# Kernel tuning notes

Measured on AMD Instinct MI355X. Metric: run time of the kernel, lower is better.

The kernel has to match this reference:

```python
import jax, jax.numpy as jnp
import numpy as np

N = 1147      # 240 lncRNA + 412 disease + 495 miRNA nodes (hard-coded in source)
HID = 512
NH = 8        # heads
P = 73408     # edges (avg degree ~64)
IN_CH = 512


def _ln(x, eps=1e-5):
    m = x.mean(-1, keepdims=True)
    v = ((x - m) ** 2).mean(-1, keepdims=True)
    return (x - m) * jax.lax.rsqrt(v + eps)


def _seg_softmax_agg(logits, v_src, dst, n):
    # logits: [P, NH], v_src: [P, NH, d]; softmax over incoming edges per dst node
    m = jax.ops.segment_max(logits, dst, num_segments=n)
    m = jnp.where(jnp.isfinite(m), m, 0.0)
    a = jnp.exp(logits - m[dst])
    den = jax.ops.segment_sum(a, dst, num_segments=n)
    w = a / (den[dst] + 1e-9)
    return jax.ops.segment_sum(w[..., None] * v_src, dst, num_segments=n)


def _lap_pe(src, dst, n, k):
    # symmetric normalized Laplacian eigenvector positional encoding
    A = jnp.zeros((n, n), jnp.float32).at[src, dst].set(1.0)
    A = jnp.maximum(A, A.T)
    dinv = jax.lax.rsqrt(jnp.maximum(A.sum(1), 1.0))
    L = jnp.eye(n, dtype=jnp.float32) - dinv[:, None] * A * dinv[None, :]
    _, vecs = jnp.linalg.eigh(L)
    return vecs[:, 1:k + 1]  # drop trivial eigenvector


def _edge_layer(h, e, src, dst, Wq, Wk, Wv, We, Wo, Woe, Wfa, Wfb, Wea, Web):
    n, D = h.shape
    d = D // NH
    scale = 1.0 / np.sqrt(d)
    q = (h @ Wq).reshape(n, NH, d)
    k = (h @ Wk).reshape(n, NH, d)
    v = (h @ Wv).reshape(n, NH, d)
    ep = (e @ We).reshape(-1, NH, d)
    score = k[src] * q[dst] * scale * ep           # [P, NH, d]
    e1 = _ln(e + score.reshape(-1, D) @ Woe)       # edge residual path
    e1 = _ln(e1 + jax.nn.relu(e1 @ Wea) @ Web)
    agg = _seg_softmax_agg(score.sum(-1), v[src], dst, n).reshape(n, D)
    h1 = _ln(h + agg @ Wo)
    h1 = _ln(h1 + jax.nn.relu(h1 @ Wfa) @ Wfb)
    return h1, e1


def _gt_layer(h, src, dst, Wq, Wk, Wv, Wo, Wfa, Wfb):
    n, D = h.shape
    d = D // NH
    scale = 1.0 / np.sqrt(d)
    q = (h @ Wq).reshape(n, NH, d)
    k = (h @ Wk).reshape(n, NH, d)
    v = (h @ Wv).reshape(n, NH, d)
    logits = (k[src] * q[dst]).sum(-1) * scale     # [P, NH]
    agg = _seg_softmax_agg(logits, v[src], dst, n).reshape(n, D)
    h1 = _ln(h + agg @ Wo)
    h1 = _ln(h1 + jax.nn.relu(h1 @ Wfa) @ Wfb)
    return h1


def setup_inputs() -> dict:
    key = jax.random.key(0)
    ks = jax.random.split(key, 32)
    s = 0.02
    w = lambda i, shp: jax.random.normal(ks[i], shp, jnp.float32) * s
    return {
        'H': jax.random.normal(ks[0], (N, 1147), jnp.float32),
        'edge_w': jax.random.uniform(ks[1], (P, 1), jnp.float32),
        'edge_src': jax.random.randint(ks[2], (P,), 0, N, jnp.int32),
        'edge_dst': jax.random.randint(ks[3], (P,), 0, N, jnp.int32),
        'W_lin': w(4, (1147, IN_CH)), 'b_lin': jnp.zeros((IN_CH,), jnp.float32),
        'W_e': w(5, (1, HID)), 'b_e': jnp.zeros((HID,), jnp.float32),
        'W_h': w(6, (IN_CH, HID)), 'b_h': jnp.zeros((HID,), jnp.float32),
        'W_lap': w(7, (HID, HID)), 'b_lap': jnp.zeros((HID,), jnp.float32),
        'Wq1': w(8, (HID, HID)), 'Wk1': w(9, (HID, HID)), 'Wv1': w(10, (HID, HID)),
        'We1': w(11, (HID, HID)), 'Wo1': w(12, (HID, HID)), 'Woe1': w(13, (HID, HID)),
        'Wf1a': w(14, (HID, 2 * HID)), 'Wf1b': w(15, (2 * HID, HID)),
        'We1a': w(16, (HID, 2 * HID)), 'We1b': w(17, (2 * HID, HID)),
        'Wq2': w(18, (HID, HID)), 'Wk2': w(19, (HID, HID)), 'Wv2': w(20, (HID, HID)),
        'Wo2': w(21, (HID, HID)),
        'Wf2a': w(22, (HID, 2 * HID)), 'Wf2b': w(23, (2 * HID, HID)),
    }


def reference(H, edge_w, W_lin, b_lin, W_e, b_e, W_h, b_h, W_lap, b_lap,
              Wq1, Wk1, Wv1, We1, Wo1, Woe1, Wf1a, Wf1b, We1a, We1b,
              Wq2, Wk2, Wv2, Wo2, Wf2a, Wf2b, edge_src, edge_dst):
    e = edge_w @ W_e + b_e                       # embedding_e on edge weights
    h = (H @ W_lin + b_lin) @ W_h + b_h          # linear(1147->in_ch) then embedding_h
    pe = _lap_pe(edge_src, edge_dst, N, HID)     # laplacian positional encoding
    h = h + pe @ W_lap + b_lap
    z, _ = _edge_layer(h, e, edge_src, edge_dst, Wq1, Wk1, Wv1, We1,
                       Wo1, Woe1, Wf1a, Wf1b, We1a, We1b)
    z = _gt_layer(z, edge_src, edge_dst, Wq2, Wk2, Wv2, Wo2, Wf2a, Wf2b)
    return z  # [N, HID], already flat per node
```

## Files before the change

kernel.cpp:

```cpp
#include <hip/hip_runtime.h>
#include <hip/hip_cooperative_groups.h>
#include <math.h>

#define NN 1147
#define HID 512
#define LDAe 1152
#define LDQ 1152
#define LDD 1147
#define EPS32 5.9604644775390625e-08f
#define SAFMIN32 1.17549435e-38f
#define I0E 1026
#define TGRID 64
#define TBLK 1024

struct EDMeta { int K; int nrot; int early; float rho; };
struct ETree { int st[64]; int sz[64]; int cnt; };
struct MergeLvl { int cnt; int st[32]; int n1[32]; int n2[32]; };

__device__ __forceinline__ float lapy2f(float x, float y){
  float xa=fabsf(x), ya=fabsf(y), w=fmaxf(xa,ya), z2=fminf(xa,ya);
  if (z2==0.f) return w;
  float q=z2/w; return w*sqrtf(1.f+q*q);
}
__device__ __forceinline__ void slartg(float ff, float gg, float* c, float* s, float* r){
  if (gg==0.f){ *c=1.f; *s=0.f; *r=ff; }
  else if (ff==0.f){ *c=0.f; *s=copysignf(1.f,gg); *r=fabsf(gg); }
  else {
    float d=sqrtf(ff*ff+gg*gg);
    *c=fabsf(ff)/d;
    *r=copysignf(d,ff);
    *s=gg/(*r);
  }
}
__device__ void slaev2(float a, float b, float cc, float* rt1, float* rt2, float* cs1, float* sn1){
  float sm=a+cc, df=a-cc, adf=fabsf(df), tb=b+b, ab=fabsf(tb);
  float acmx, acmn;
  if (fabsf(a)>fabsf(cc)){ acmx=a; acmn=cc; } else { acmx=cc; acmn=a; }
  float rt;
  if (adf>ab) rt=adf*sqrtf(1.f+(ab/adf)*(ab/adf));
  else if (adf<ab) rt=ab*sqrtf(1.f+(adf/ab)*(adf/ab));
  else rt=ab*sqrtf(2.f);
  int sgn1;
  if (sm<0.f){ *rt1=0.5f*(sm-rt); sgn1=-1; *rt2=(acmx/(*rt1))*acmn-(b/(*rt1))*b; }
  else if (sm>0.f){ *rt1=0.5f*(sm+rt); sgn1=1; *rt2=(acmx/(*rt1))*acmn-(b/(*rt1))*b; }
  else { *rt1=0.5f*rt; *rt2=-0.5f*rt; sgn1=1; }
  int sgn2; float cs;
  if (df>=0.f){ cs=df+rt; sgn2=1; } else { cs=df-rt; sgn2=-1; }
  float acs=fabsf(cs);
  if (acs>ab){ float ct=-tb/cs; *sn1=1.f/sqrtf(1.f+ct*ct); *cs1=ct*(*sn1); }
  else {
    if (ab==0.f){ *cs1=1.f; *sn1=0.f; }
    else { float tn=-cs/tb; *cs1=1.f/sqrtf(1.f+tn*tn); *sn1=tn*(*cs1); }
  }
  if (sgn1==sgn2){ float tn=*cs1; *cs1=-(*sn1); *sn1=tn; }
}
__device__ void lamrg0(int n1,int n2,const float* a,int dtrd1,int dtrd2,int* idx){
  int n1sv=n1,n2sv=n2;
  int ind1=(dtrd1>0)?0:(n1-1);
  int ind2=(dtrd2>0)?n1:(n1+n2-1);
  int i=0;
  while(n1sv>0&&n2sv>0){
    if(a[ind1]<=a[ind2]){idx[i++]=ind1;ind1+=dtrd1;n1sv--;}
    else{idx[i++]=ind2;ind2+=dtrd2;n2sv--;}
  }
  while(n2sv>0){idx[i++]=ind2;ind2+=dtrd2;n2sv--;}
  while(n1sv>0){idx[i++]=ind1;ind1+=dtrd1;n1sv--;}
}

__global__ __launch_bounds__(256) void k_zero_f(float* p, int n){
  int i = blockIdx.x*256+threadIdx.x; if (i<n) p[i]=0.f;
}
__global__ __launch_bounds__(256) void k_zero_i(int* p, int n){
  int i = blockIdx.x*256+threadIdx.x; if (i<n) p[i]=0;
}

__global__ __launch_bounds__(256) void k_adj(const int* __restrict__ src, const int* __restrict__ dst,
                                             float* __restrict__ A, int P){
  int p = blockIdx.x*256+threadIdx.x;
  if (p>=P) return;
  int s=src[p], d=dst[p];
  A[(size_t)s*LDAe+d]=1.f;
  A[(size_t)d*LDAe+s]=1.f;
}
__global__ __launch_bounds__(256) void k_deg(const float* __restrict__ A, float* __restrict__ dinv){
  int row=blockIdx.x; int tid=threadIdx.x;
  __shared__ float red[256];
  float s=0.f;
  for (int c=tid;c<NN;c+=256) s+=A[(size_t)row*LDAe+c];
  red[tid]=s; __syncthreads();
  for(int st=128;st;st>>=1){ if(tid<st) red[tid]+=red[tid+st]; __syncthreads(); }
  if(tid==0) dinv[row]=1.f/sqrtf(fmaxf(red[0],1.f));
}
__global__ __launch_bounds__(256) void k_lap(float* __restrict__ A, const float* __restrict__ dinv){
  int row=blockIdx.y; int col=blockIdx.x*256+threadIdx.x;
  if (col>=NN) return;
  size_t idx=(size_t)row*LDAe+col;
  float v=A[idx];
  float v1=(dinv[row]*v)*dinv[col];
  float v2=(dinv[col]*v)*dinv[row];
  A[idx] = ((row==col)?1.f:0.f) - 0.5f*(v1+v2);
}

__device__ __forceinline__ float dload(const float* p){
  return __hip_atomic_load(p, __ATOMIC_RELAXED, __HIP_MEMORY_SCOPE_AGENT);
}
__device__ __forceinline__ void dstore(float* p, float v){
  __hip_atomic_store(p, v, __ATOMIC_RELAXED, __HIP_MEMORY_SCOPE_AGENT);
}

__device__ __forceinline__ void gbar(unsigned* flags, unsigned* gen, unsigned tgt){
  __syncthreads();
  if (threadIdx.x==0)
    __hip_atomic_store(&flags[blockIdx.x], tgt, __ATOMIC_RELAXED, __HIP_MEMORY_SCOPE_AGENT);
  if (blockIdx.x==0){
    if (threadIdx.x<TGRID){
      while (__hip_atomic_load(&flags[threadIdx.x], __ATOMIC_RELAXED, __HIP_MEMORY_SCOPE_AGENT) < tgt)
        __builtin_amdgcn_s_sleep(1);
    }
    __syncthreads();
    if (threadIdx.x==0)
      __hip_atomic_store(gen, tgt, __ATOMIC_RELAXED, __HIP_MEMORY_SCOPE_AGENT);
  } else {
    if (threadIdx.x==0){
      while (__hip_atomic_load(gen, __ATOMIC_RELAXED, __HIP_MEMORY_SCOPE_AGENT) < tgt)
        __builtin_amdgcn_s_sleep(1);
    }
    __syncthreads();
  }
}

__global__ __launch_bounds__(1024) void k_trid(float* __restrict__ A, float* __restrict__ evec,
    float* __restrict__ tauv, float* __restrict__ scalv, float* __restrict__ pv2,
    float* __restrict__ pub4, unsigned* __restrict__ flags, unsigned* __restrict__ gen){
  __shared__ float vbuf[2][1152];
  __shared__ float pcur[1152];
  __shared__ float pubc[1152];
  __shared__ float red[256];
  int tid=threadIdx.x, bid=blockIdx.x;
  int wv=tid>>6, lane=tid&63;
  unsigned tgt=0;
  float tau, scal;
  {
    const float* row0=A;
    int m0=NN-1;
    if (tid<256){
      float s=0.f;
      for(int t=tid;t<m0-1;t+=256){ float x=row0[2+t]; s+=x*x; }
      red[tid]=s;
    }
    __syncthreads();
    for(int st=128;st;st>>=1){ if(tid<st) red[tid]+=red[tid+st]; __syncthreads(); }
    float alpha=row0[1], xn2=red[0];
    float beta;
    if(xn2==0.f){ tau=0.f; beta=alpha; scal=0.f; }
    else { beta=-copysignf(sqrtf(alpha*alpha+xn2),alpha); tau=(beta-alpha)/beta; scal=1.f/(alpha-beta); }
    if(bid==0&&tid==0){ evec[0]=beta; tauv[0]=tau; scalv[0]=scal; }
    __syncthreads();
    for(int t=tid;t<m0;t+=TBLK) vbuf[0][t]=row0[1+t];
    __syncthreads();
    for(int rr=0;rr<2;rr++){
      int r=16*bid+wv+rr*1024;
      if(r<1||r>=NN) continue;
      const float* arow=A+(size_t)r*LDAe+1;
      float acc=0.f;
      for(int c=lane;c<m0;c+=64){
        float v=(c==0)?1.f:vbuf[0][c]*scal;
        acc+=arow[c]*v;
      }
      for(int o=32;o;o>>=1) acc+=__shfl_down(acc,o,64);
      if(lane==0) dstore(&pv2[r],acc);
    }
    if(bid==0&&wv==1){
      const float* r1=A+(size_t)LDAe;
      for(int c=2+lane;c<NN;c+=64) dstore(&pub4[1280+c],r1[c]);
    }
  }
  gbar(flags,gen,++tgt);
  int cur=0;
  for(int i=0;i<I0E;i++){
    int m=NN-1-i, mp=m-1;
    float* vcur=vbuf[cur]; float* nxt=vbuf[cur^1];
    const float* pvs=pv2+(size_t)(i&1)*1280;
    const float* pbs=pub4+(size_t)((i+1)&3)*1280;
    for(int t=tid;t<m;t+=TBLK){
      pcur[t]=dload(&pvs[(i+1)+t]);
      if(t<mp) pubc[t]=dload(&pbs[(i+2)+t]);
    }
    __syncthreads();
    if (tid<256){
      float s=0.f;
      for(int t=tid;t<m;t+=256){ float v=(t==0)?1.f:vcur[t]*scal; s+=pcur[t]*v; }
      red[tid]=s;
    }
    __syncthreads();
    for(int st=128;st;st>>=1){ if(tid<st) red[tid]+=red[tid+st]; __syncthreads(); }
    float c2=tau*tau*red[0]*0.5f;
    __syncthreads();
    const float vz=1.f;
    float wR0=tau*pcur[0]-c2*vz;
    for(int t=tid;t<mp;t+=TBLK){
      float vC=vcur[1+t]*scal;
      float wC=tau*pcur[1+t]-c2*vC;
      nxt[t]=pubc[t]-(vz*wC+wR0*vC);
    }
    __syncthreads();
    if (tid<256){
      float s2=0.f;
      for(int t=tid;t<mp-1;t+=256){ float x=nxt[1+t]; s2+=x*x; }
      red[tid]=s2;
    }
    __syncthreads();
    for(int st=128;st;st>>=1){ if(tid<st) red[tid]+=red[tid+st]; __syncthreads(); }
    float alpha1=nxt[0], xn2=red[0];
    float beta1,tau1,scal1;
    if(xn2==0.f){ tau1=0.f; beta1=alpha1; scal1=0.f; }
    else { beta1=-copysignf(sqrtf(alpha1*alpha1+xn2),alpha1); tau1=(beta1-alpha1)/beta1; scal1=1.f/(alpha1-beta1); }
    if(bid==0&&tid==0){ evec[i+1]=beta1; tauv[i+1]=tau1; scalv[i+1]=scal1; }
    __syncthreads();
    float* pvd=pv2+(size_t)((i+1)&1)*1280;
    float* pbd=pub4+(size_t)((i+2)&3)*1280;
    for(int rr=0;rr<2;rr++){
      int r=16*bid+wv+rr*1024;
      if(r<i+1||r>=NN) continue;
      int tr=r-(i+1);
      float vR=(tr==0)?1.f:vcur[tr]*scal;
      float wR=tau*pcur[tr]-c2*vR;
      float* arow=A+(size_t)r*LDAe;
      if(lane==0) arow[i+1]=arow[i+1]-(vR*wR0+wR*vz);
      if(tr==0){
        for(int c=lane;c<mp;c+=64) arow[i+2+c]=nxt[c];
      } else {
        float acc=0.f;
        int ispub=(tr==1);
        for(int c=lane;c<mp;c+=64){
          float vC=vcur[1+c]*scal;
          float wC=tau*pcur[1+c]-c2*vC;
          float val=arow[i+2+c]-(vR*wC+wR*vC);
          arow[i+2+c]=val;
          float v1=(c==0)?1.f:nxt[c]*scal1;
          acc+=val*v1;
          if(ispub) dstore(&pbd[(i+2)+c],val);
        }
        for(int o=32;o;o>>=1) acc+=__shfl_down(acc,o,64);
        if(lane==0) dstore(&pvd[r],acc);
      }
    }
    gbar(flags,gen,++tgt);
    cur^=1; tau=tau1; scal=scal1;
  }
}
__global__ __launch_bounds__(256) void k_tend(float* __restrict__ A, float* __restrict__ evec,
    float* __restrict__ tauv, float* __restrict__ scalv){
  __shared__ float T[121][122];
  __shared__ float red[256];
  __shared__ float pl[121];
  __shared__ float el[121], tl[121], sl[121];
  __shared__ float sh3[2];
  int tid=threadIdx.x;
  for(int e=tid;e<121*121;e+=256){ int r=e/121,c=e%121; T[r][c]=A[(size_t)(I0E+r)*LDAe + I0E+c]; }
  __syncthreads();
  for(int li=0; li<120; ++li){
    int m=120-li;
    float s=0.f;
    for(int t=tid;t<m-1;t+=256){ float x=T[li][li+2+t]; s+=x*x; }
    red[tid]=s; __syncthreads();
    for(int st=128;st;st>>=1){ if(tid<st) red[tid]+=red[tid+st]; __syncthreads(); }
    if(tid==0){
      float alpha=T[li][li+1], xn2=red[0];
      float beta,tau,scal;
      if(xn2==0.f){ tau=0.f; beta=alpha; scal=0.f; }
      else { beta=-copysignf(sqrtf(alpha*alpha+xn2),alpha); tau=(beta-alpha)/beta; scal=1.f/(alpha-beta); }
      el[li]=beta; tl[li]=tau; sl[li]=scal;
      sh3[0]=tau; sh3[1]=scal;
    }
    __syncthreads();
    float tau=sh3[0], scal=sh3[1];
    if(tid<m){
      float acc=0.f;
      for(int c=0;c<m;c++){
        float v=(c==0)?1.f:T[li][li+1+c]*scal;
        acc+=T[li+1+tid][li+1+c]*v;
      }
      pl[tid]=acc;
    }
    __syncthreads();
    s=0.f;
    for(int t=tid;t<m;t+=256){
      float v=(t==0)?1.f:T[li][li+1+t]*scal;
      s+=pl[t]*v;
    }
    red[tid]=s; __syncthreads();
    for(int st=128;st;st>>=1){ if(tid<st) red[tid]+=red[tid+st]; __syncthreads(); }
    float c2=tau*tau*red[0]*0.5f;
    for(int e=tid;e<m*m;e+=256){
      int r=e/m, c=e%m;
      float vR=(r==0)?1.f:T[li][li+1+r]*scal;
      float vC=(c==0)?1.f:T[li][li+1+c]*scal;
      float wR=tau*pl[r]-c2*vR;
      float wC=tau*pl[c]-c2*vC;
      T[li+1+r][li+1+c]-=vR*wC+wR*vC;
    }
    __syncthreads();
  }
  for(int e=tid;e<121*121;e+=256){ int r=e/121,c=e%121; A[(size_t)(I0E+r)*LDAe + I0E+c]=T[r][c]; }
  for(int t=tid;t<120;t+=256){ evec[I0E+t]=el[t]; tauv[I0E+t]=tl[t]; scalv[I0E+t]=sl[t]; }
}
__global__ __launch_bounds__(256) void k_harvest(const float* __restrict__ A, float* __restrict__ dv){
  int t=blockIdx.x*256+threadIdx.x;
  if (t<NN) dv[t]=A[(size_t)t*LDAe+t];
}

__global__ __launch_bounds__(256) void k_ed_scale(float* __restrict__ D, float* __restrict__ E){
  __shared__ float red[256];
  int tid=threadIdx.x;
  float m=0.f;
  for(int i=tid;i<NN;i+=256) m=fmaxf(m,fabsf(D[i]));
  for(int i=tid;i<NN-1;i+=256) m=fmaxf(m,fabsf(E[i]));
  red[tid]=m; __syncthreads();
  for(int s=128;s;s>>=1){ if(tid<s) red[tid]=fmaxf(red[tid],red[tid+s]); __syncthreads(); }
  float mul=1.f/red[0];
  __syncthreads();
  for(int i=tid;i<NN;i+=256) D[i]*=mul;
  for(int i=tid;i<NN-1;i+=256) E[i]*=mul;
}
__global__ void k_ed_cuts(float* D, const float* E, ETree t){
  int b=threadIdx.x;
  if (b==0||b>=t.cnt) return;
  int cut=t.st[b];
  float ae=fabsf(E[cut-1]);
  D[cut-1]-=ae; D[cut]-=ae;
// ... 63 lines not shown
        }
        for(int j2=mm-1;j2>=l;j2--){
          float cc=workc[j2-l], ss2=works[j2-l];
          if (cc!=1.f||ss2!=0.f)
            for(int row=lane;row<n;row+=64){
              float t1=z[(size_t)(j2+1)*ldz+row];
              z[(size_t)(j2+1)*ldz+row]=cc*t1 - ss2*z[(size_t)j2*ldz+row];
              z[(size_t)j2*ldz+row]=ss2*t1 + cc*z[(size_t)j2*ldz+row];
            }
        }
        d[l]=d[l]-p;
        e[l]=g;
      }
    } else {
      for(;;){
        int mm;
        for(mm=l;mm>lend;mm--){
          float tst=e[mm-1]*e[mm-1];
          if (tst<=(eps2*fabsf(d[mm]))*fabsf(d[mm-1])+safmin) break;
        }
        if (mm>lend) e[mm-1]=0.f;
        p=d[l];
        if (mm==l){ d[l]=p; l--; if (l>=lend) continue; else break; }
        if (mm==l-1){
          slaev2(d[l-1],e[l-1],d[l],&rt1,&rt2,&c,&s);
          for(int row=lane;row<n;row+=64){
            float t1=z[(size_t)l*ldz+row];
            z[(size_t)l*ldz+row]=c*t1 - s*z[(size_t)(l-1)*ldz+row];
            z[(size_t)(l-1)*ldz+row]=s*t1 + c*z[(size_t)(l-1)*ldz+row];
          }
          d[l-1]=rt1; d[l]=rt2; e[l-1]=0.f;
          l-=2;
          if (l>=lend) continue; else break;
        }
        if (jtot==nmaxit) break;
        jtot++;
        g=(d[l-1]-p)/(2.f*e[l-1]);
        r=lapy2f(g,1.f);
        g=d[mm]-p+(e[l-1]/(g+copysignf(r,g)));
        s=1.f; c=1.f; p=0.f;
        for(int i=mm;i<=l-1;i++){
          f=s*e[i]; b=c*e[i];
          slartg(g,f,&c,&s,&r);
          if (i!=mm) e[i-1]=r;
          g=d[i]-p;
          r=(d[i+1]-g)*s+2.f*c*b;
          p=s*r;
          d[i]=g+p;
          g=c*r-b;
          workc[i-mm]=c; works[i-mm]=s;
        }
        for(int j2=mm;j2<=l-1;j2++){
          float cc=workc[j2-mm], ss2=works[j2-mm];
          if (cc!=1.f||ss2!=0.f)
            for(int row=lane;row<n;row+=64){
              float t1=z[(size_t)(j2+1)*ldz+row];
              z[(size_t)(j2+1)*ldz+row]=cc*t1 - ss2*z[(size_t)j2*ldz+row];
              z[(size_t)j2*ldz+row]=ss2*t1 + cc*z[(size_t)j2*ldz+row];
            }
        }
        d[l]=d[l]-p;
        e[l-1]=g;
      }
    }
  }
  for(int ii=1;ii<n;ii++){
    int i=ii-1,k=i; float pp=d[i];
    for(int j2=ii;j2<n;j2++) if (d[j2]<pp){k=j2;pp=d[j2];}
    if (k!=i){
      d[k]=d[i]; d[i]=pp;
      for(int row=lane;row<n;row+=64){
        float t1=z[(size_t)i*ldz+row];
        z[(size_t)i*ldz+row]=z[(size_t)k*ldz+row];
        z[(size_t)k*ldz+row]=t1;
      }
    }
  }
}
__global__ __launch_bounds__(64) void k_ed_leaves(float* D, float* E, float* QM, int* indxq, ETree t){
  int lf=blockIdx.x;
  if (lf>=t.cnt) return;
  int lane=threadIdx.x;
  int st=t.st[lf], n=t.sz[lf];
  float* z=QM+(size_t)st*LDQ+st;
  for(int c=lane;c<n;c+=64) z[(size_t)c*LDQ+c]=1.f;
  steqr1w(n, D+st, E+st, z, LDQ, lane);
  for(int i=lane;i<n;i+=64) indxq[st+i]=i;
}

__global__ __launch_bounds__(256) void k_ed_deflate2(float* __restrict__ D, int* __restrict__ indxq,
    float* __restrict__ dlamda, float* __restrict__ w, float* __restrict__ dstage,
    int* __restrict__ colmap, int* __restrict__ cmtype, int* __restrict__ indxcg,
    int* __restrict__ rotp, int* __restrict__ rotn, float* __restrict__ rotc, float* __restrict__ rots,
    EDMeta* __restrict__ meta, const float* __restrict__ QM, const float* __restrict__ E, MergeLvl lv){
  int mid=blockIdx.x; if(mid>=lv.cnt) return;
  int st=lv.st[mid], n1=lv.n1[mid], n2=lv.n2[mid], n=n1+n2;
  int tid=threadIdx.x;
  __shared__ float zl[1152], dl_[1152], dlam[1152], wl[1152], ds2[1152];
  __shared__ int iq[1152], im[1152], ix[1152], ixp[1152], ict[1152], is2[1152];
  __shared__ float rv[256]; __shared__ int ri[256];
  __shared__ float srho; __shared__ int sK, snrot, searly, simax, sjmax;
  float rr=E[st+n1-1];
  if(tid==0) srho=fabsf(2.f*rr);
  for(int i=tid;i<n;i+=256){
    float v = (i<n1)? QM[(size_t)(st+i)*LDQ + st+n1-1] : QM[(size_t)(st+i)*LDQ + st+n1];
    if(rr<0.f && i>=n1) v=-v;
    zl[i]=v*0.70710678118654752440f;
    dl_[i]=D[st+i];
    int q=indxq[st+i]; if(i>=n1) q+=n1;
    iq[i]=q;
    ict[i]=(i<n1)?1:3;
  }
  __syncthreads();
  {
    float bv=-1.f; int bi=0;
    for(int i2=tid;i2<n;i2+=256){ float a=fabsf(zl[i2]); if(a>bv){bv=a;bi=i2;} }
    rv[tid]=bv; ri[tid]=bi; __syncthreads();
    for(int stp=128;stp;stp>>=1){
      if(tid<stp){ if(rv[tid+stp]>rv[tid]||(rv[tid+stp]==rv[tid]&&ri[tid+stp]<ri[tid])){rv[tid]=rv[tid+stp];ri[tid]=ri[tid+stp];} }
      __syncthreads();
    }
    if(tid==0) simax=ri[0];
    __syncthreads();
  }
  {
    float bv=-1.f; int bi=0;
    for(int i2=tid;i2<n;i2+=256){ float a=fabsf(dl_[i2]); if(a>bv){bv=a;bi=i2;} }
    rv[tid]=bv; ri[tid]=bi; __syncthreads();
    for(int stp=128;stp;stp>>=1){
      if(tid<stp){ if(rv[tid+stp]>rv[tid]||(rv[tid+stp]==rv[tid]&&ri[tid+stp]<ri[tid])){rv[tid]=rv[tid+stp];ri[tid]=ri[tid+stp];} }
      __syncthreads();
    }
    if(tid==0) sjmax=ri[0];
    __syncthreads();
  }
  if(tid==0){
    for(int i=0;i<n;i++) dlam[i]=dl_[iq[i]];
    lamrg0(n1,n2,dlam,1,1,im);
    for(int i=0;i<n;i++) ix[i]=iq[im[i]];
    float tol=8.f*EPS32*fmaxf(fabsf(dl_[sjmax]),fabsf(zl[simax]));
    float rho=srho;
    int K=0,nrot=0,early=0;
    if(rho*fabsf(zl[simax])<=tol){
      early=1;
      for(int i=0;i<n;i++){ int s2=ix[i]; im[i]=s2; iq[i]=2; ds2[i]=dl_[s2]; is2[i]=i; }
    } else {
      int K2=n; int pj=0; int j=0;
      for(;j<n;j++){ int nj=ix[j]; if(rho*fabsf(zl[nj])<=tol){K2--;ict[nj]=4;ixp[K2]=nj;} else {pj=nj;break;} }
      for(j=j+1;;j++){
        if(j>=n) break;
        int nj=ix[j];
        if(rho*fabsf(zl[nj])<=tol){K2--;ict[nj]=4;ixp[K2]=nj;}
        else {
          float s=zl[pj], c=zl[nj];
          float tau2=lapy2f(c,s);
          float t=dl_[nj]-dl_[pj];
          c=c/tau2; s=-s/tau2;
          if(fabsf(t*c*s)<=tol){
            zl[nj]=tau2; zl[pj]=0.f;
            if(ict[nj]!=ict[pj]) ict[nj]=2;
            ict[pj]=4;
            rotp[st+nrot]=pj; rotn[st+nrot]=nj; rotc[st+nrot]=c; rots[st+nrot]=s; nrot++;
            float t2=dl_[pj]*c*c + dl_[nj]*s*s;
            dl_[nj]=dl_[pj]*s*s + dl_[nj]*c*c;
            dl_[pj]=t2;
            K2--;
            int i2=1;
            for(;;){
              if(K2+i2<=n-1 && dl_[pj]<dl_[ixp[K2+i2]]){ ixp[K2+i2-1]=ixp[K2+i2]; ixp[K2+i2]=pj; i2++; }
              else { ixp[K2+i2-1]=pj; break; }
// ... 196 lines not shown
  int mid=blockIdx.y; if(mid>=lv.cnt) return;
  int st=lv.st[mid];
  int K=meta[mid].K;
  int j=blockIdx.x; if (j>=K) return;
  float* dcol=DC+(size_t)(st+j)*LDD;
  const int* indxc=indxcg+st;
  int tid=threadIdx.x;
  if (K==1){ if (tid==0) dcol[0]=1.f; return; }
  if (K==2){
    if (tid==0){
      float a=dcol[0], b=dcol[1];
      float o0=(indxc[0]==0)?a:b;
      float o1=(indxc[1]==0)?a:b;
      dcol[0]=o0; dcol[1]=o1;
    }
    return;
  }
  __shared__ float sv[1152];
  __shared__ double red[256];
  double ss=0.0;
  for(int i=tid;i<K;i+=256){
    float s=w[st+i]/dcol[i];
    sv[i]=s;
    ss+=(double)s*(double)s;
  }
  red[tid]=ss; __syncthreads();
  for(int st2=128;st2;st2>>=1){ if(tid<st2) red[tid]+=red[tid+st2]; __syncthreads(); }
  float tempf=(float)sqrt(red[0]);
  __syncthreads();
  for(int i=tid;i<K;i+=256) dcol[i]=sv[indxc[i]]/tempf;
}
__global__ __launch_bounds__(256) void k_gemm_cm2(const float* __restrict__ Q2, const float* __restrict__ DC,
    float* __restrict__ QM, const EDMeta* __restrict__ meta, MergeLvl lv){
  int mid=blockIdx.z; if(mid>=lv.cnt) return;
  int st=lv.st[mid], n=lv.n1[mid]+lv.n2[mid];
  int K=meta[mid].K;
  int br=blockIdx.x*64, bj=blockIdx.y*64;
  if (br>=n||bj>=n) return;
  int tid=threadIdx.x, tr=tid/16, tc=tid%16;
  if (bj>=K){
    for(int i=0;i<4;i++){ int r=br+tr*4+i; if(r>=n)continue;
      for(int j2=0;j2<4;j2++){ int cc=bj+tc*4+j2; if(cc>=n)continue;
        QM[(size_t)(st+cc)*LDQ+st+r]=Q2[(size_t)(st+cc)*LDQ+st+r]; } }
    return;
  }
  __shared__ float As[16][65], Bs[16][65];
  float acc[4][4]={};
  for(int k0=0;k0<K;k0+=16){
    for(int l=0;l<4;l++){
      int e2=tid+l*256;
      int rr=e2&63, ii=e2>>6;
      float av=0.f;
      if (br+rr<n && k0+ii<K) av=Q2[(size_t)(st+k0+ii)*LDQ + st+br+rr];
      As[ii][rr]=av;
      int bi=e2&15, bj2=e2>>4;
      float bv=0.f;
      if (k0+bi<K && bj+bj2<n) bv=DC[(size_t)(st+bj+bj2)*LDD + k0+bi];
      Bs[bi][bj2]=bv;
    }
    __syncthreads();
    #pragma unroll
    for(int kk=0;kk<16;kk++){
      float ar[4],br2[4];
      #pragma unroll
      for(int i=0;i<4;i++) ar[i]=As[kk][tr*4+i];
      #pragma unroll
      for(int j2=0;j2<4;j2++) br2[j2]=Bs[kk][tc*4+j2];
      #pragma unroll
      for(int i=0;i<4;i++)
        #pragma unroll
        for(int j2=0;j2<4;j2++) acc[i][j2]+=ar[i]*br2[j2];
    }
    __syncthreads();
  }
  for(int i=0;i<4;i++){
    int r=br+tr*4+i; if (r>=n) continue;
    for(int j2=0;j2<4;j2++){
      int cc=bj+tc*4+j2; if (cc>=n) continue;
      if (cc<K) QM[(size_t)(st+cc)*LDQ + st+r]=acc[i][j2];
      else      QM[(size_t)(st+cc)*LDQ + st+r]=Q2[(size_t)(st+cc)*LDQ + st+r];
    }
  }
}
__global__ void k_ed_post(float* __restrict__ D, const float* __restrict__ dstage,
    int* __restrict__ indxq, const EDMeta* __restrict__ meta, MergeLvl lv){
  int mid=blockIdx.x; if(mid>=lv.cnt||threadIdx.x!=0) return;
  int st=lv.st[mid], n=lv.n1[mid]+lv.n2[mid];
  int K=meta[mid].K;
  float* Ds=D+st; int* ixq=indxq+st;
  for(int i=K;i<n;i++) Ds[i]=dstage[st+i];
  if (meta[mid].early){ for(int i=0;i<n;i++) ixq[i]=i; return; }
  lamrg0(K, n-K, Ds, 1, -1, ixq);
}
__global__ __launch_bounds__(256) void k_ed_gather(const float* __restrict__ QM, const int* __restrict__ indxq,
    float* __restrict__ Vt){
  int row=blockIdx.x*256+threadIdx.x;
  int vec=blockIdx.y;
  if (row>=NN) return;
  int src=indxq[vec+1];
  Vt[(size_t)vec*NN+row]=QM[(size_t)src*LDQ+row];
}

__global__ __launch_bounds__(256) void k_backt(const float* __restrict__ A, const float* __restrict__ tauv,
                                               const float* __restrict__ scalv, float* __restrict__ Vt){
  int wv=threadIdx.x>>6, lane=threadIdx.x&63;
  int vec=blockIdx.x*4+wv;
  float* col=Vt+(size_t)vec*NN;
  for(int i=NN-2;i>=0;i--){
    float tau=tauv[i];
    if (tau==0.f) continue;
    int m=NN-1-i;
    float scal=scalv[i];
    const float* rowi=A+(size_t)i*LDAe;
    float s=0.f;
    for(int t=lane;t<m;t+=64){
      float v=(t==0)?1.f:rowi[i+1+t]*scal;
      s+=v*col[i+1+t];
    }
    for(int o=32;o;o>>=1) s+=__shfl_down(s,o,64);
    s=__shfl(s,0,64);
    s*=tau;
    for(int t=lane;t<m;t+=64){
      float v=(t==0)?1.f:rowi[i+1+t]*scal;
      col[i+1+t]-=s*v;
    }
  }
}

__global__ __launch_bounds__(256) void k_transpose(const float* __restrict__ in, float* __restrict__ outp){
  __shared__ float tile[32][33];
  int c0=blockIdx.x*32, r0=blockIdx.y*32;
  int tx=threadIdx.x%32, ty=threadIdx.x/32;
  for(int s=0;s<32;s+=8){
    int r=r0+ty+s, c=c0+tx;
    tile[ty+s][tx]=(r<512 && c<NN)? in[(size_t)r*NN+c] : 0.f;
  }
  __syncthreads();
  for(int s=0;s<32;s+=8){
    int r=c0+ty+s, c=r0+tx;
    if (r<NN && c<512) outp[(size_t)r*512+c]=tile[tx][ty+s];
  }
}

__global__ __launch_bounds__(256) void k_gemm(const float* __restrict__ A, const float* __restrict__ B,
    const float* __restrict__ bias, const float* __restrict__ add, float* __restrict__ C,
    int M, int Nc, int K, int relu){
  __shared__ float As[16][65];
  __shared__ float Bs[16][65];
  int bm=blockIdx.y*64, bn=blockIdx.x*64;
  int tid=threadIdx.x;
  int tr=tid/16, tc=tid%16;
  float acc[4][4]={};
  for(int k0=0;k0<K;k0+=16){
    for(int l=0;l<4;l++){
      int e2=tid+l*256;
      int m_=e2/16, kk=e2%16;
      float av=0.f;
      if (bm+m_<M && k0+kk<K) av=A[(size_t)(bm+m_)*K + k0+kk];
      As[kk][m_]=av;
      int k2=e2/64, n2=e2%64;
      float bv=0.f;
      if (k0+k2<K && bn+n2<Nc) bv=B[(size_t)(k0+k2)*Nc + bn+n2];
      Bs[k2][n2]=bv;
    }
    __syncthreads();
    for(int kk=0;kk<16;kk++){
      float ar[4], br[4];
      #pragma unroll
      for(int i=0;i<4;i++) ar[i]=As[kk][tr*4+i];
      #pragma unroll
      for(int j=0;j<4;j++) br[j]=Bs[kk][tc*4+j];
      #pragma unroll
      for(int i=0;i<4;i++)
        #pragma unroll
        for(int j=0;j<4;j++) acc[i][j]+=ar[i]*br[j];
    }
    __syncthreads();
  }
  for(int i=0;i<4;i++){
    int r=bm+tr*4+i;
    if (r>=M) continue;
    for(int j=0;j<4;j++){
      int c=bn+tc*4+j;
      if (c>=Nc) continue;
      float x=acc[i][j];
      if (bias) x+=bias[c];
      if (add)  x+=add[(size_t)r*Nc+c];
      if (relu) x=fmaxf(x,0.f);
      C[(size_t)r*Nc+c]=x;
    }
  }
}

__global__ __launch_bounds__(256) void k_lnadd(const float* __restrict__ x, const float* __restrict__ y,
                                               float* __restrict__ out){
  int row=blockIdx.x; int tid=threadIdx.x;
  __shared__ float red[256];
  size_t base=(size_t)row*HID;
  float v0=x[base+tid]+y[base+tid];
  float v1=x[base+256+tid]+y[base+256+tid];
  red[tid]=v0+v1; __syncthreads();
  for(int st=128;st;st>>=1){ if(tid<st) red[tid]+=red[tid+st]; __syncthreads(); }
  float mean=red[0]*(1.f/512.f);
  __syncthreads();
  float d0=v0-mean, d1=v1-mean;
  red[tid]=d0*d0+d1*d1; __syncthreads();
  for(int st=128;st;st>>=1){ if(tid<st) red[tid]+=red[tid+st]; __syncthreads(); }
  float r=rsqrtf(red[0]*(1.f/512.f)+1e-5f);
  out[base+tid]=d0*r;
  out[base+256+tid]=d1*r;
}

__global__ __launch_bounds__(256) void k_prep_uw(const float* __restrict__ We, const float* __restrict__ be,
    const float* __restrict__ We1, float* __restrict__ u, float* __restrict__ w1){
  int c=blockIdx.x*256+threadIdx.x;
  if (c>=HID) return;
  float a=0.f,b=0.f;
  for(int f=0;f<HID;f++){ float m=We1[(size_t)f*HID+c]; a+=We[f]*m; b+=be[f]*m; }
  u[c]=a; w1[c]=b;
}

__global__ __launch_bounds__(256) void k_elogits(const float* __restrict__ q, const float* __restrict__ kk,
    const int* __restrict__ src, const int* __restrict__ dst, const float* __restrict__ ew,
    const float* __restrict__ uu, const float* __restrict__ ww, float* __restrict__ logit, int P, int useep){
  int gw=(blockIdx.x*256+threadIdx.x)>>6;
  int lane=threadIdx.x&63;
  if (gw>=P) return;
  int s=src[gw], d=dst[gw];
  const float* kr=kk+(size_t)s*HID;
  const float* qr=q+(size_t)d*HID;
  float a1[8], a2[8];
  #pragma unroll
  for(int j=0;j<8;j++){
    int c=j*64+lane;
    float prod=kr[c]*qr[c];
    if (useep){ a1[j]=prod*uu[c]; a2[j]=prod*ww[c]; }
    else { a1[j]=prod; a2[j]=0.f; }
  }
  #pragma unroll
  for(int o=32;o;o>>=1){
    #pragma unroll
    for(int j=0;j<8;j++){ a1[j]+=__shfl_down(a1[j],o,64); a2[j]+=__shfl_down(a2[j],o,64); }
  }
  if (lane==0){
    float w0 = useep? ew[gw] : 0.f;
    #pragma unroll
    for(int j=0;j<8;j++){
      float lg = useep ? 0.125f*(w0*a1[j]+a2[j]) : 0.125f*a1[j];
      logit[(size_t)gw*8+j]=lg;
    }
  }
}

__global__ __launch_bounds__(256) void k_count(const int* __restrict__ dst, int* __restrict__ cnt, int P){
  int p=blockIdx.x*256+threadIdx.x;
  if (p<P) atomicAdd(&cnt[dst[p]],1);
}
__global__ void k_scan(const int* __restrict__ cnt, int* __restrict__ iptr){
  int s=0; iptr[0]=0;
  for(int n=0;n<NN;n++){ s+=cnt[n]; iptr[n+1]=s; }
}
__global__ __launch_bounds__(256) void k_fill(const int* __restrict__ dst, const int* __restrict__ iptr,
                                              int* __restrict__ iidx, int P){
  int n=blockIdx.x; int tid=threadIdx.x;
  int lane=tid&63, wv=tid>>6;
  __shared__ int wb[4]; __shared__ int scnt;
  if (tid==0) scnt=iptr[n];
  __syncthreads();
  for(int base=0;base<P;base+=256){
    int p=base+tid;
    bool f=(p<P)&&(dst[p]==n);
    unsigned long long m=__ballot(f);
    if (lane==0) wb[wv]=__popcll(m);
    __syncthreads();
    int off=0;
    #pragma unroll
    for(int i=0;i<4;i++) if (i<wv) off+=wb[i];
    if (f){
      int pre=__popcll(m & ((1ull<<lane)-1ull));
      iidx[scnt+off+pre]=p;
    }
    int tot=wb[0]+wb[1]+wb[2]+wb[3];
    __syncthreads();
    if (tid==0) scnt+=tot;
    __syncthreads();
  }
}

__global__ __launch_bounds__(256) void k_softmax(const float* __restrict__ logit, const int* __restrict__ iptr,
    const int* __restrict__ iidx, float* __restrict__ wght){
  int n=blockIdx.x; int tid=threadIdx.x;
  int beg=iptr[n], end=iptr[n+1];
  if (beg==end) return;
  __shared__ float red[256];
  __shared__ float smax[8], sden[8];
  float mx[8];
  #pragma unroll
  for(int h=0;h<8;h++) mx[h]=-1e30f;
  for(int t=beg+tid;t<end;t+=256){
    int e=iidx[t];
    #pragma unroll
    for(int h=0;h<8;h++) mx[h]=fmaxf(mx[h],logit[(size_t)e*8+h]);
  }
  for(int h=0;h<8;h++){
    red[tid]=mx[h]; __syncthreads();
    for(int st=128;st;st>>=1){ if(tid<st) red[tid]=fmaxf(red[tid],red[tid+st]); __syncthreads(); }
    if (tid==0) smax[h]=red[0];
    __syncthreads();
  }
  float sm[8];
  #pragma unroll
  for(int h=0;h<8;h++) sm[h]=0.f;
  for(int t=beg+tid;t<end;t+=256){
    int e=iidx[t];
    #pragma unroll
    for(int h=0;h<8;h++) sm[h]+=expf(logit[(size_t)e*8+h]-smax[h]);
  }
  for(int h=0;h<8;h++){
    red[tid]=sm[h]; __syncthreads();
    for(int st=128;st;st>>=1){ if(tid<st) red[tid]+=red[tid+st]; __syncthreads(); }
    if (tid==0) sden[h]=red[0];
    __syncthreads();
  }
  for(int t=beg+tid;t<end;t+=256){
    int e=iidx[t];
    #pragma unroll
    for(int h=0;h<8;h++) wght[(size_t)e*8+h]=expf(logit[(size_t)e*8+h]-smax[h])/(sden[h]+1e-9f);
  }
}

__global__ __launch_bounds__(512) void k_agg(const float* __restrict__ wght, const float* __restrict__ vv,
    const int* __restrict__ src, const int* __restrict__ iptr, const int* __restrict__ iidx,
    float* __restrict__ agg){
  int n=blockIdx.x; int c=threadIdx.x; int h=c>>6;
  int beg=iptr[n], end=iptr[n+1];
  float acc=0.f;
  for(int t=beg;t<end;++t){
    int e=iidx[t];
    acc += wght[(size_t)e*8+h]*vv[(size_t)src[e]*HID+c];
  }
  agg[(size_t)n*HID+c]=acc;
}

extern "C" void kernel_launch(void* const* d_in, const int* in_sizes, int n_in,
                              void* d_out, int out_size, void* d_ws, size_t ws_size,
                              hipStream_t stream){
  const float* H      = (const float*)d_in[0];
  const float* edge_w = (const float*)d_in[1];
  const int*   esrc   = (const int*)d_in[2];
  const int*   edst   = (const int*)d_in[3];
  const float* W_lin  = (const float*)d_in[4];
  const float* b_lin  = (const float*)d_in[5];
  const float* W_e    = (const float*)d_in[6];
  const float* b_e    = (const float*)d_in[7];
  const float* W_h    = (const float*)d_in[8];
  const float* b_h    = (const float*)d_in[9];
  const float* W_lap  = (const float*)d_in[10];
  const float* b_lap  = (const float*)d_in[11];
  const float* Wq1    = (const float*)d_in[12];
  const float* Wk1    = (const float*)d_in[13];
  const float* Wv1    = (const float*)d_in[14];
  const float* We1    = (const float*)d_in[15];
  const float* Wo1    = (const float*)d_in[16];
  const float* Wf1a   = (const float*)d_in[18];
  const float* Wf1b   = (const float*)d_in[19];
  const float* Wq2    = (const float*)d_in[22];
  const float* Wk2    = (const float*)d_in[23];
  const float* Wv2    = (const float*)d_in[24];
  const float* Wo2    = (const float*)d_in[25];
  const float* Wf2a   = (const float*)d_in[26];
  const float* Wf2b   = (const float*)d_in[27];
  const int P = in_sizes[1];
  float* out = (float*)d_out;

  char* base=(char*)d_ws;
  size_t off=0;
  auto AF=[&](size_t n)->float*{ float* r=(float*)(base+off); off+=((n*4+255)/256)*256; return r; };
  auto AI=[&](size_t n)->int*{ int* r=(int*)(base+off); off+=((n*4+255)/256)*256; return r; };
  const size_t SLOT=(size_t)NN*HID;
  float* A   = AF((size_t)NN*LDAe);
  float* QM  = AF((size_t)LDQ*NN);
  float* Q2  = AF((size_t)LDQ*NN);
  float* DC  = AF((size_t)LDD*LDD);
  float* dvec  = AF(1280);
  float* evec  = AF(1280);
  float* tauv  = AF(1280);
  float* scalv = AF(1280);
  float* pvec  = AF(1280);
  float* eddl  = AF(1280);
  float* edw   = AF(1280);
  float* edds  = AF(1280);
  float* rotc  = AF(1280);
  float* rots  = AF(1280);
  float* ub    = AF(512);
  float* w1b   = AF(512);
  float* pv2   = AF(2*1280);
  float* pub4  = AF(4*1280);
  int* indxq=AI(1280); int* edcm=AI(1280); int* edcmt=AI(1280); int* edic=AI(1280);
  int* rotp=AI(1280); int* rotn=AI(1280);
  EDMeta* meta=(EDMeta*)AI(192);
  int* icnt=AI(NN); int* iptr=AI(NN+1); int* iidx=AI(P);
  int* barws=AI(512);
  unsigned* flags=(unsigned*)barws;
  unsigned* gen=(unsigned*)(barws+256);
  (void)ws_size; (void)n_in; (void)out_size;

  float* W0=A;        float* W1=A+SLOT;
  float* W2=QM;       float* W3=QM+SLOT;
  float* W4=Q2;       float* W5=Q2+SLOT;
  float* W6=DC;       float* W7=DC+SLOT;
  (void)W7;
  float* Vt=W6;
  float* pe=W2;

  auto GEMM=[&](const float*Am,const float*Bm,const float*bias,const float*add,float*C,int M,int Nc,int K,int relu){
    dim3 g((Nc+63)/64,(M+63)/64);
    k_gemm<<<g,256,0,stream>>>(Am,Bm,bias,add,C,M,Nc,K,relu);
  };

  {
    int ntot=NN*LDAe;
    k_zero_f<<<(ntot+255)/256,256,0,stream>>>(A,ntot);
    k_adj<<<(P+255)/256,256,0,stream>>>(esrc,edst,A,P);
    k_deg<<<NN,256,0,stream>>>(A,pvec);
    dim3 g((NN+255)/256,NN);
    k_lap<<<g,256,0,stream>>>(A,pvec);
  }
  k_zero_i<<<2,256,0,stream>>>(barws,512);
  {
    void* kargs[] = { (void*)&A, (void*)&evec, (void*)&tauv, (void*)&scalv,
                      (void*)&pv2, (void*)&pub4, (void*)&flags, (void*)&gen };
    hipLaunchCooperativeKernel((const void*)k_trid, dim3(TGRID), dim3(TBLK), kargs, 0, stream);
  }
  k_tend<<<1,256,0,stream>>>(A,evec,tauv,scalv);
  k_harvest<<<(NN+255)/256,256,0,stream>>>(A,dvec);

  ETree tr;
  {
    int tmp[64]; tmp[0]=NN; int cnt=1;
    while (tmp[cnt-1]>25){
      for(int j2=cnt-1;j2>=0;j2--){ int p=tmp[j2]; tmp[2*j2]=p/2; tmp[2*j2+1]=p-p/2; }
      cnt*=2;
    }
    tr.cnt=cnt;
    int acc=0;
    for(int j2=0;j2<cnt;j2++){ tr.st[j2]=acc; tr.sz[j2]=tmp[j2]; acc+=tmp[j2]; }
  }
  k_ed_scale<<<1,256,0,stream>>>(dvec,evec);
  k_zero_f<<<(LDQ*NN+255)/256,256,0,stream>>>(QM,LDQ*NN);
  k_ed_cuts<<<1,64,0,stream>>>(dvec,evec,tr);
  k_ed_leaves<<<tr.cnt,64,0,stream>>>(dvec,evec,QM,indxq,tr);

  {
    int csz[64], cst[64], cn=tr.cnt;
    for(int i=0;i<cn;i++){ csz[i]=tr.sz[i]; cst[i]=tr.st[i]; }
    while (cn>1){
      MergeLvl lv; lv.cnt=cn/2;
      int maxn=0;
      for(int i=0;i<cn/2;i++){
        lv.st[i]=cst[2*i]; lv.n1[i]=csz[2*i]; lv.n2[i]=csz[2*i+1];
        int n=lv.n1[i]+lv.n2[i]; if(n>maxn) maxn=n;
      }
      k_ed_deflate2<<<lv.cnt,256,0,stream>>>(dvec,indxq,eddl,edw,edds,edcm,edcmt,edic,
                                             rotp,rotn,rotc,rots,meta,QM,evec,lv);
      { dim3 gr((maxn+255)/256,lv.cnt);
        k_ed_rot2<<<gr,256,0,stream>>>(QM,rotp,rotn,rotc,rots,meta,lv); }
      { dim3 gp((maxn+255)/256,maxn,lv.cnt);
        k_ed_permute<<<gp,256,0,stream>>>(QM,Q2,edcm,edcmt,lv); }
      { dim3 gs((maxn+63)/64,lv.cnt);
        k_ed_secular<<<gs,64,0,stream>>>(eddl,edw,meta,dvec,DC,lv);
        k_ed_lowner<<<gs,64,0,stream>>>(eddl,edw,DC,meta,lv); }
      { dim3 gv(maxn,lv.cnt);
        k_ed_vecs<<<gv,256,0,stream>>>(edw,DC,edic,meta,lv); }
      { dim3 gg((maxn+63)/64,(maxn+63)/64,lv.cnt);
        k_gemm_cm2<<<gg,256,0,stream>>>(Q2,DC,QM,meta,lv); }
      k_ed_post<<<lv.cnt,1,0,stream>>>(dvec,edds,indxq,meta,lv);
      for(int i=0;i<cn/2;i++){ cst[i]=cst[2*i]; csz[i]=csz[2*i]+csz[2*i+1]; }
      cn>>=1;
    }
  }
  { dim3 gg((NN+255)/256,512); k_ed_gather<<<gg,256,0,stream>>>(QM,indxq,Vt); }
  k_backt<<<128,256,0,stream>>>(A,tauv,scalv,Vt);
  { dim3 g((NN+31)/32,(512+31)/32); k_transpose<<<g,256,0,stream>>>(Vt,pe); }

  float* hx=W0; float* h0=W1; float* hb=W4;
  GEMM(H,W_lin,b_lin,nullptr,hx,NN,HID,NN,0);
  GEMM(hx,W_h,b_h,nullptr,h0,NN,HID,HID,0);
  GEMM(pe,W_lap,b_lap,h0,hb,NN,HID,HID,0);
  k_prep_uw<<<2,256,0,stream>>>(W_e,b_e,We1,ub,w1b);
  k_zero_i<<<(NN+255)/256,256,0,stream>>>(icnt,NN);
  k_count<<<(P+255)/256,256,0,stream>>>(edst,icnt,P);
  k_scan<<<1,1,0,stream>>>(icnt,iptr);
  k_fill<<<NN,256,0,stream>>>(edst,iptr,iidx,P);
  float* qb=W0; float* kb=W1; float* vb=W3;
  GEMM(hb,Wq1,nullptr,nullptr,qb,NN,HID,HID,0);
  GEMM(hb,Wk1,nullptr,nullptr,kb,NN,HID,HID,0);
  GEMM(hb,Wv1,nullptr,nullptr,vb,NN,HID,HID,0);
  float* logit=W2;
  k_elogits<<<(P+3)/4,256,0,stream>>>(qb,kb,esrc,edst,edge_w,ub,w1b,logit,P,1);
  float* wght=W5;
  k_softmax<<<NN,256,0,stream>>>(logit,iptr,iidx,wght);
  float* aggb=W6;
  k_agg<<<NN,512,0,stream>>>(wght,vb,esrc,iptr,iidx,aggb);
  float* ob=W0;
  GEMM(aggb,Wo1,nullptr,nullptr,ob,NN,HID,HID,0);
  float* h1a=W3;
  k_lnadd<<<NN,256,0,stream>>>(hb,ob,h1a);
  float* tb1=W0;
  GEMM(h1a,Wf1a,nullptr,nullptr,tb1,NN,1024,HID,1);
  float* fb=W2;
  GEMM(tb1,Wf1b,nullptr,nullptr,fb,NN,HID,1024,0);
  float* h1=W5;
  k_lnadd<<<NN,256,0,stream>>>(h1a,fb,h1);
  float* q2=W0; float* k2=W1; float* v2=W2;
  GEMM(h1,Wq2,nullptr,nullptr,q2,NN,HID,HID,0);
  GEMM(h1,Wk2,nullptr,nullptr,k2,NN,HID,HID,0);
  GEMM(h1,Wv2,nullptr,nullptr,v2,NN,HID,HID,0);
  float* logit2=W3;
  k_elogits<<<(P+3)/4,256,0,stream>>>(q2,k2,esrc,edst,nullptr,nullptr,nullptr,logit2,P,0);
  float* wght2=W4;
  k_softmax<<<NN,256,0,stream>>>(logit2,iptr,iidx,wght2);
  float* agg2=W6;
  k_agg<<<NN,512,0,stream>>>(wght2,v2,esrc,iptr,iidx,agg2);
  float* o2=W0;
  GEMM(agg2,Wo2,nullptr,nullptr,o2,NN,HID,HID,0);
  float* h2a=W1;
  k_lnadd<<<NN,256,0,stream>>>(h1,o2,h2a);
  float* tb2=W2;
  GEMM(h2a,Wf2a,nullptr,nullptr,tb2,NN,1024,HID,1);
  float* f2=W0;
  GEMM(tb2,Wf2b,nullptr,nullptr,f2,NN,HID,1024,0);
  k_lnadd<<<NN,256,0,stream>>>(h2a,f2,out);
}
```

Baseline: 30.63 ms.

## Replicate barrier generation flags, fuse tridiagonal-loop phases, stage small kernels in LDS

The grid barrier now gives each block its own padded copy of the generation counter, so 63 blocks no longer poll one shared address. In the tridiagonalization loop, the loads of the p-vector are fused into the dot-product reduction and the next-vector update is fused into the norm reduction, which removes two __syncthreads per iteration. The leaf eigensolver, the merge post-step and the CSR scan now stage their data in shared memory and use more threads for loads and stores. The main risk is extra barrier traffic from writing 64 flags, and the leaf kernel's 32-entry buffers assume leaves no larger than 32.

Result: no change. 30.82 ms (+0.6%).

```diff
diff --git a/kernel.cpp b/kernel.cpp
--- a/kernel.cpp
+++ b/kernel.cpp
@@ -12,6 +12,7 @@
 #define I0E 1026
 #define TGRID 64
 #define TBLK 1024
+#define GENSTRIDE 16
 
 struct EDMeta { int K; int nrot; int early; float rho; };
 struct ETree { int st[64]; int sz[64]; int cnt; };
@@ -108,7 +109,7 @@
   __hip_atomic_store(p, v, __ATOMIC_RELAXED, __HIP_MEMORY_SCOPE_AGENT);
 }
 
-__device__ __forceinline__ void gbar(unsigned* flags, unsigned* gen, unsigned tgt){
+__device__ __forceinline__ void gbar(unsigned* flags, unsigned* genrep, unsigned tgt){
   __syncthreads();
   if (threadIdx.x==0)
     __hip_atomic_store(&flags[blockIdx.x], tgt, __ATOMIC_RELAXED, __HIP_MEMORY_SCOPE_AGENT);
@@ -118,11 +119,11 @@
         __builtin_amdgcn_s_sleep(1);
     }
     __syncthreads();
-    if (threadIdx.x==0)
-      __hip_atomic_store(gen, tgt, __ATOMIC_RELAXED, __HIP_MEMORY_SCOPE_AGENT);
+    if (threadIdx.x<TGRID)
+      __hip_atomic_store(&genrep[threadIdx.x*GENSTRIDE], tgt, __ATOMIC_RELAXED, __HIP_MEMORY_SCOPE_AGENT);
   } else {
     if (threadIdx.x==0){
-      while (__hip_atomic_load(gen, __ATOMIC_RELAXED, __HIP_MEMORY_SCOPE_AGENT) < tgt)
+      while (__hip_atomic_load(&genrep[blockIdx.x*GENSTRIDE], __ATOMIC_RELAXED, __HIP_MEMORY_SCOPE_AGENT) < tgt)
         __builtin_amdgcn_s_sleep(1);
     }
     __syncthreads();
@@ -131,7 +132,7 @@
 
 __global__ __launch_bounds__(1024) void k_trid(float* __restrict__ A, float* __restrict__ evec,
     float* __restrict__ tauv, float* __restrict__ scalv, float* __restrict__ pv2,
-    float* __restrict__ pub4, unsigned* __restrict__ flags, unsigned* __restrict__ gen){
+    float* __restrict__ pub4, unsigned* __restrict__ flags, unsigned* __restrict__ genrep){
   __shared__ float vbuf[2][1152];
   __shared__ float pcur[1152];
   __shared__ float pubc[1152];
@@ -175,22 +176,24 @@
       for(int c=2+lane;c<NN;c+=64) dstore(&pub4[1280+c],r1[c]);
     }
   }
-  gbar(flags,gen,++tgt);
+  gbar(flags,genrep,++tgt);
   int cur=0;
   for(int i=0;i<I0E;i++){
     int m=NN-1-i, mp=m-1;
     float* vcur=vbuf[cur]; float* nxt=vbuf[cur^1];
     const float* pvs=pv2+(size_t)(i&1)*1280;
     const float* pbs=pub4+(size_t)((i+1)&3)*1280;
-    for(int t=tid;t<m;t+=TBLK){
-      pcur[t]=dload(&pvs[(i+1)+t]);
-      if(t<mp) pubc[t]=dload(&pbs[(i+2)+t]);
-    }
-    __syncthreads();
     if (tid<256){
       float s=0.f;
-      for(int t=tid;t<m;t+=256){ float v=(t==0)?1.f:vcur[t]*scal; s+=pcur[t]*v; }
+      for(int t=tid;t<m;t+=256){
+        float pv=dload(&pvs[(i+1)+t]);
+        pcur[t]=pv;
+        float v=(t==0)?1.f:vcur[t]*scal;
+        s+=pv*v;
+      }
       red[tid]=s;
+    } else {
+      for(int t=tid-256;t<mp;t+=768) pubc[t]=dload(&pbs[(i+2)+t]);
     }
     __syncthreads();
     for(int st=128;st;st>>=1){ if(tid<st) red[tid]+=red[tid+st]; __syncthreads(); }
@@ -198,15 +201,20 @@
     __syncthreads();
     const float vz=1.f;
     float wR0=tau*pcur[0]-c2*vz;
-    for(int t=tid;t<mp;t+=TBLK){
-      float vC=vcur[1+t]*scal;
-      float wC=tau*pcur[1+t]-c2*vC;
-      nxt[t]=pubc[t]-(vz*wC+wR0*vC);
-    }
-    __syncthreads();
     if (tid<256){
       float s2=0.f;
-      for(int t=tid;t<mp-1;t+=256){ float x=nxt[1+t]; s2+=x*x; }
+      if (tid==0){
+        float vC=vcur[1]*scal;
+        float wC=tau*pcur[1]-c2*vC;
+        nxt[0]=pubc[0]-(vz*wC+wR0*vC);
+      }
+      for(int u=tid+1;u<mp;u+=256){
+        float vC=vcur[1+u]*scal;
+        float wC=tau*pcur[1+u]-c2*vC;
+        float x=pubc[u]-(vz*wC+wR0*vC);
+        nxt[u]=x;
+        s2+=x*x;
+      }
       red[tid]=s2;
     }
     __syncthreads();
@@ -245,7 +253,7 @@
         if(lane==0) dstore(&pvd[r],acc);
       }
     }
-    gbar(flags,gen,++tgt);
+    gbar(flags,genrep,++tgt);
     cur^=1; tau=tau1; scal=scal1;
   }
 }
@@ -475,10 +483,16 @@
   if (lf>=t.cnt) return;
   int lane=threadIdx.x;
   int st=t.st[lf], n=t.sz[lf];
+  __shared__ float dl[32], el[32];
+  for(int i=lane;i<n;i+=64) dl[i]=D[st+i];
+  for(int i=lane;i<n-1;i+=64) el[i]=E[st+i];
+  __syncthreads();
   float* z=QM+(size_t)st*LDQ+st;
   for(int c=lane;c<n;c+=64) z[(size_t)c*LDQ+c]=1.f;
-  steqr1w(n, D+st, E+st, z, LDQ, lane);
-  for(int i=lane;i<n;i+=64) indxq[st+i]=i;
+  steqr1w(n, dl, el, z, LDQ, lane);
+  __syncthreads();
+  for(int i=lane;i<n;i+=64){ D[st+i]=dl[i]; indxq[st+i]=i; }
+  for(int i=lane;i<n-1;i+=64) E[st+i]=el[i];
 }
 
 __global__ __launch_bounds__(256) void k_ed_deflate2(float* __restrict__ D, int* __restrict__ indxq,
@@ -841,15 +855,28 @@
     }
   }
 }
-__global__ void k_ed_post(float* __restrict__ D, const float* __restrict__ dstage,
+__global__ __launch_bounds__(256) void k_ed_post(float* __restrict__ D, const float* __restrict__ dstage,
     int* __restrict__ indxq, const EDMeta* __restrict__ meta, MergeLvl lv){
-  int mid=blockIdx.x; if(mid>=lv.cnt||threadIdx.x!=0) return;
+  int mid=blockIdx.x; if(mid>=lv.cnt) return;
   int st=lv.st[mid], n=lv.n1[mid]+lv.n2[mid];
   int K=meta[mid].K;
-  float* Ds=D+st; int* ixq=indxq+st;
-  for(int i=K;i<n;i++) Ds[i]=dstage[st+i];
-  if (meta[mid].early){ for(int i=0;i<n;i++) ixq[i]=i; return; }
-  lamrg0(K, n-K, Ds, 1, -1, ixq);
+  int tid=threadIdx.x;
+  __shared__ float dl[1152];
+  __shared__ int iq[1152];
+  float* Ds=D+st;
+  for(int i=tid;i<n;i+=256){
+    float v = (i<K)? Ds[i] : dstage[st+i];
+    dl[i]=v;
+    if (i>=K) Ds[i]=v;
+  }
+  __syncthreads();
+  if (meta[mid].early){
+    for(int i=tid;i<n;i+=256) indxq[st+i]=i;
+    return;
+  }
+  if (tid==0) lamrg0(K, n-K, dl, 1, -1, iq);
+  __syncthreads();
+  for(int i=tid;i<n;i+=256) indxq[st+i]=iq[i];
 }
 __global__ __launch_bounds__(256) void k_ed_gather(const float* __restrict__ QM, const int* __restrict__ indxq,
     float* __restrict__ Vt){
@@ -1015,9 +1042,18 @@
   int p=blockIdx.x*256+threadIdx.x;
   if (p<P) atomicAdd(&cnt[dst[p]],1);
 }
-__global__ void k_scan(const int* __restrict__ cnt, int* __restrict__ iptr){
-  int s=0; iptr[0]=0;
-  for(int n=0;n<NN;n++){ s+=cnt[n]; iptr[n+1]=s; }
+__global__ __launch_bounds__(256) void k_scan(const int* __restrict__ cnt, int* __restrict__ iptr){
+  __shared__ int c[NN+1];
+  int tid=threadIdx.x;
+  for(int i=tid;i<NN;i+=256) c[i]=cnt[i];
+  __syncthreads();
+  if (tid==0){
+    int s=0;
+    for(int n=0;n<NN;n++){ int t=c[n]; c[n]=s; s+=t; }
+    c[NN]=s;
+  }
+  __syncthreads();
+  for(int i=tid;i<=NN;i+=256) iptr[i]=c[i];
 }
 __global__ __launch_bounds__(256) void k_fill(const int* __restrict__ dst, const int* __restrict__ iptr,
                                               int* __restrict__ iidx, int P){
@@ -1159,9 +1195,9 @@
   int* rotp=AI(1280); int* rotn=AI(1280);
   EDMeta* meta=(EDMeta*)AI(192);
   int* icnt=AI(NN); int* iptr=AI(NN+1); int* iidx=AI(P);
-  int* barws=AI(512);
+  int* barws=AI(2048);
   unsigned* flags=(unsigned*)barws;
-  unsigned* gen=(unsigned*)(barws+256);
+  unsigned* genrep=(unsigned*)(barws+64);
   (void)ws_size; (void)n_in; (void)out_size;
 
   float* W0=A;        float* W1=A+SLOT;
@@ -1185,10 +1221,10 @@
     dim3 g((NN+255)/256,NN);
     k_lap<<<g,256,0,stream>>>(A,pvec);
   }
-  k_zero_i<<<2,256,0,stream>>>(barws,512);
+  k_zero_i<<<8,256,0,stream>>>(barws,2048);
   {
     void* kargs[] = { (void*)&A, (void*)&evec, (void*)&tauv, (void*)&scalv,
-                      (void*)&pv2, (void*)&pub4, (void*)&flags, (void*)&gen };
+                      (void*)&pv2, (void*)&pub4, (void*)&flags, (void*)&genrep };
     hipLaunchCooperativeKernel((const void*)k_trid, dim3(TGRID), dim3(TBLK), kargs, 0, stream);
   }
   k_tend<<<1,256,0,stream>>>(A,evec,tauv,scalv);
@@ -1233,7 +1269,7 @@
         k_ed_vecs<<<gv,256,0,stream>>>(edw,DC,edic,meta,lv); }
       { dim3 gg((maxn+63)/64,(maxn+63)/64,lv.cnt);
         k_gemm_cm2<<<gg,256,0,stream>>>(Q2,DC,QM,meta,lv); }
-      k_ed_post<<<lv.cnt,1,0,stream>>>(dvec,edds,indxq,meta,lv);
+      k_ed_post<<<lv.cnt,256,0,stream>>>(dvec,edds,indxq,meta,lv);
       for(int i=0;i<cn/2;i++){ cst[i]=cst[2*i]; csz[i]=csz[2*i]+csz[2*i+1]; }
       cn>>=1;
     }
@@ -1249,7 +1285,7 @@
   k_prep_uw<<<2,256,0,stream>>>(W_e,b_e,We1,ub,w1b);
   k_zero_i<<<(NN+255)/256,256,0,stream>>>(icnt,NN);
   k_count<<<(P+255)/256,256,0,stream>>>(edst,icnt,P);
-  k_scan<<<1,1,0,stream>>>(icnt,iptr);
+  k_scan<<<1,256,0,stream>>>(icnt,iptr);
   k_fill<<<NN,256,0,stream>>>(edst,iptr,iidx,P);
   float* qb=W0; float* kb=W1; float* vb=W3;
   GEMM(hb,Wq1,nullptr,nullptr,qb,NN,HID,HID,0);
```
